# Kernel tuning notes

Measured on AMD Instinct MI355X. Metric: run time of the kernel, lower is better.

The kernel has to match this reference:

```python
import jax, jax.numpy as jnp
import numpy as np

W = 10        # hurst window == signature path window (increments)
DELTA_MAX = 1.5
BN_EPS = 1e-5


def _revcumsum(x, axis):
    return jnp.flip(jnp.cumsum(jnp.flip(x, axis), axis=axis), axis)


def _forward(features, hw1, hb1, hw2, hb2, hw3, hb3, gw1, gb1, gw2, gb2,
             p1, p1b, p2, p2b, p3, p3b, p4, p4b,
             w1, b1, gamma, beta, rmean, rvar, w2, b2, w3, b3):
    B, T, d = features.shape
    f32 = features.dtype
    # log returns, left-padded with 0
    lp = features[:, :, 0]
    ret = jnp.pad(lp[:, 1:] - lp[:, :-1], ((0, 0), (1, 0)))
    # Hurst estimator on sliding windows returns[:, t-W:t] for t in [W, T)
    idxh = jnp.arange(T - W)[:, None] + jnp.arange(W)[None, :]
    rw = ret[:, idxh]                                          # [B, T-W, W]
    hh = jax.nn.relu(rw @ hw1 + hb1)
    hh = jax.nn.relu(hh @ hw2 + hb2)
    H_tail = 0.5 * jax.nn.sigmoid((hh @ hw3 + hb3)[..., 0])    # [B, T-W]
    # first W entries copy the t=W estimate (matches torch slice-broadcast)
    H_local = jnp.concatenate([jnp.repeat(H_tail[:, :1], W, axis=1), H_tail], axis=1)
    vol = jnp.cumsum(jnp.abs(ret), axis=1) / (jnp.arange(1, T + 1, dtype=f32) + 1e-8)
    # depth gate from (H_local, vol_local)
    regime = jnp.stack([H_local, vol], axis=-1)                # [B, T, 2]
    gate = jax.nn.softmax(jax.nn.relu(regime @ gw1 + gb1) @ gw2 + gb2, axis=-1)  # [B,T,4]
    # windowed path increments: window at t covers global increments t-W .. t-1
    Dinc = features[:, 1:] - features[:, :-1]                  # [B, T-1, d]
    Dp = jnp.pad(Dinc, ((0, 0), (W, 0), (0, 0)))
    idx = jnp.arange(T)[:, None] + jnp.arange(W)[None, :]
    Dw = Dp[:, idx]                                            # [B, T, W, d] (zero-padded early)
    S = _revcumsum(Dw, 2)                                      # suffix sums S_r = sum_{m>=r} D_m
    lvl1 = S[:, :, 0]                                          # [B, T, d] = path[-1]-path[0]
    # level2 (torch loop) = sum_{i<=m} D_i (x) D_m  (diagonal included)
    A = Dw[..., :, None] * S[..., None, :]                     # [B, T, W, d, d]
    l2f = jnp.sum(A, axis=2).reshape(B, T, d * d)
    # level3 (torch loop) = sum_{i<j<=n} D_i (x) D_j (x) D_n
    RA = _revcumsum(A, 2) - A                                  # exclusive suffix sum of A
    l3f = jnp.einsum('btrd,btref->btdef', Dw, RA).reshape(B, T, d ** 3)
    # level4 = flatten(level2 (x) level2); (d^2)^2 == d^4 so no pad/trunc
    l4f = (l2f[..., :, None] * l2f[..., None, :]).reshape(B, T, d ** 4)
    proj1 = lvl1 @ p1 + p1b
    proj2 = jnp.concatenate([lvl1, l2f], -1) @ p2 + p2b
    proj3 = jnp.concatenate([lvl1, l2f, l3f], -1) @ p3 + p3b
    proj4 = jnp.concatenate([lvl1, l2f, l3f, l4f], -1) @ p4 + p4b
    # depth k active iff path_len >= k+1 i.e. t >= k (k = depth index)
    tv = jnp.arange(T)
    m2 = (tv >= 1).astype(f32)[None, :, None]
    m3 = (tv >= 2).astype(f32)[None, :, None]
    m4 = (tv >= 3).astype(f32)[None, :, None]
    sig_repr = (gate[..., 0:1] * proj1 + m2 * gate[..., 1:2] * proj2
                + m3 * gate[..., 2:3] * proj3 + m4 * gate[..., 3:4] * proj4)
    combined = jnp.concatenate([sig_repr, features], axis=-1)  # [B, T, h+d]
    h1 = jax.nn.relu(combined @ w1 + b1)
    bn = gamma * (h1 - rmean) * jax.lax.rsqrt(rvar + BN_EPS) + beta  # BatchNorm1d (eval)
    h2 = jax.nn.relu(bn @ w2 + b2)
    return DELTA_MAX * jnp.tanh((h2 @ w3 + b3)[..., 0])        # [B, T]


def setup_inputs() -> dict:
    key = jax.random.key(0)
    ks = jax.random.split(key, 24)
    B, T, d, h = 32, 2048, 5, 64
    def w(k, shape, s=0.1):
        return (jax.random.normal(k, shape) * s).astype(jnp.float32)
    z = lambda n: jnp.zeros((n,), jnp.float32)
    return dict(
        features=0.1 * jax.random.normal(ks[0], (B, T, d), jnp.float32),
        hw1=w(ks[1], (10, 32)), hb1=z(32),
        hw2=w(ks[2], (32, 32)), hb2=z(32),
        hw3=w(ks[3], (32, 1)), hb3=z(1),
        gw1=w(ks[4], (2, 32)), gb1=z(32),
        gw2=w(ks[5], (32, 4)), gb2=z(4),
        p1=w(ks[6], (5, h)), p1b=z(h),
        p2=w(ks[7], (30, h)), p2b=z(h),
        p3=w(ks[8], (155, h)), p3b=z(h),
        p4=w(ks[9], (780, h)), p4b=z(h),
        w1=w(ks[10], (h + d, h)), b1=z(h),
        gamma=jnp.ones((h,), jnp.float32), beta=z(h),
        rmean=0.05 * jax.random.normal(ks[11], (h,), dtype=jnp.float32),
        rvar=jax.random.uniform(ks[12], (h,), jnp.float32, 0.5, 1.5),
        w2=w(ks[13], (h, h // 2)), b2=z(h // 2),
        w3=w(ks[14], (h // 2, 1)), b3=z(1),
    )


def reference(features, hw1, hb1, hw2, hb2, hw3, hb3, gw1, gb1, gw2, gb2,
              p1, p1b, p2, p2b, p3, p3b, p4, p4b,
              w1, b1, gamma, beta, rmean, rvar, w2, b2, w3, b3):
    return _forward(features, hw1, hb1, hw2, hb2, hw3, hb3, gw1, gb1, gw2, gb2,
                    p1, p1b, p2, p2b, p3, p3b, p4, p4b,
                    w1, b1, gamma, beta, rmean, rvar, w2, b2, w3, b3)
```

## Files before the change

kernel.cpp:

```cpp
#include <hip/hip_runtime.h>
#include <math.h>

#define TT 2048
#define W 10

typedef short bf16x8 __attribute__((ext_vector_type(8)));
typedef float f32x4 __attribute__((ext_vector_type(4)));

#define MFMA16(a, b, c) __builtin_amdgcn_mfma_f32_16x16x32_bf16((a), (b), (c), 0, 0, 0)

__device__ __forceinline__ void splitTrunc(float v, unsigned short& hi,
                                           unsigned short& lo) {
  unsigned int u = __float_as_uint(v);
  hi = (unsigned short)(u >> 16);
  float r = v - __uint_as_float(u & 0xffff0000u);
  lo = (unsigned short)(__float_as_uint(r) >> 16);
}

__global__ __launch_bounds__(256) void prep_kernel(
    const float* __restrict__ F, const float* __restrict__ p1,
    const float* __restrict__ p2, const float* __restrict__ p3,
    const float* __restrict__ p4, unsigned short* __restrict__ WtH,
    unsigned short* __restrict__ WtL, float* __restrict__ ret,
    float* __restrict__ vol) {
  const int bid = blockIdx.x, tid = threadIdx.x;
  if (bid >= 32) {
    int g = (bid - 32) * 256 + tid;
    float v;
    if (g < 2048) {
      int h = g >> 5, k = g & 31;
      v = (k < 5) ? p1[k * 64 + h] : 0.f;
    } else if (g < 4096) {
      int loc = g - 2048, h = loc >> 5, k = loc & 31;
      v = (k < 30) ? p2[k * 64 + h] : 0.f;
    } else if (g < 14336) {
      int loc = g - 4096, h = loc / 160, k = loc - h * 160;
      v = (k < 155) ? p3[k * 64 + h] : 0.f;
    } else if (g < 24576) {
      int loc = g - 14336, h = loc / 160, k = loc - h * 160;
      v = (k < 155) ? p4[k * 64 + h] : 0.f;
    } else {
      int loc = g - 24576, row = loc >> 5, j = loc & 31;
      int i = row >> 6, h = row & 63;
      v = (j < 25) ? p4[(155 + i * 25 + j) * 64 + h] : 0.f;
    }
    unsigned short hi, lo;
    splitTrunc(v, hi, lo);
    WtH[g] = hi;
    WtL[g] = lo;
    return;
  }
  __shared__ float sAbs[TT];
  __shared__ float sPart[256];
  const float* fb = F + (size_t)bid * TT * 5;
#pragma unroll
  for (int u = 0; u < 8; ++u) {
    int t = u * 256 + tid;
    float rv = (t > 0) ? (fb[t * 5] - fb[(t - 1) * 5]) : 0.f;
    ret[bid * TT + t] = rv;
    sAbs[t] = fabsf(rv);
  }
  __syncthreads();
  float loc8[8], run = 0.f;
#pragma unroll
  for (int u = 0; u < 8; ++u) {
    run += sAbs[tid * 8 + u];
    loc8[u] = run;
  }
  sPart[tid] = run;
  __syncthreads();
  for (int off = 1; off < 256; off <<= 1) {
    float v = (tid >= off) ? sPart[tid - off] : 0.f;
    __syncthreads();
    sPart[tid] += v;
    __syncthreads();
  }
  float excl = sPart[tid] - run;
#pragma unroll
  for (int u = 0; u < 8; ++u) {
    int t = tid * 8 + u;
    vol[bid * TT + t] = (excl + loc8[u]) / ((float)(t + 1) + 1e-8f);
  }
}

__global__ __launch_bounds__(512, 2) void sig_kernel(
    const float* __restrict__ F, const float* __restrict__ ret_g,
    const float* __restrict__ vol_g, const unsigned short* __restrict__ WtH,
    const unsigned short* __restrict__ WtL, const float* __restrict__ hw1,
    const float* __restrict__ hb1, const float* __restrict__ hw2,
    const float* __restrict__ hb2, const float* __restrict__ hw3,
    const float* __restrict__ hb3, const float* __restrict__ gw1,
    const float* __restrict__ gb1, const float* __restrict__ gw2,
    const float* __restrict__ gb2, const float* __restrict__ p1b,
    const float* __restrict__ p2b, const float* __restrict__ p3b,
    const float* __restrict__ p4b, const float* __restrict__ w1,
    const float* __restrict__ b1, const float* __restrict__ gam,
    const float* __restrict__ bet, const float* __restrict__ rmean,
    const float* __restrict__ rvar, const float* __restrict__ w2,
    const float* __restrict__ b2, const float* __restrict__ w3,
    const float* __restrict__ b3, float* __restrict__ out) {
  __shared__ unsigned short phiH[32][168];
  __shared__ unsigned short phiL[32][168];
  __shared__ unsigned short l2bH[32][40];
  __shared__ unsigned short l2bL[32][40];
  __shared__ float sL2[32 * 25];
  __shared__ __align__(16) float sF[44 * 8];
  __shared__ float retl[42];
  __shared__ float voll[32];
  __shared__ float sGate[32 * 4];
  __shared__ __align__(16) float sU[4352];

  const int tid = threadIdx.x;
  const int b = blockIdx.x >> 6;
  const int t0 = (blockIdx.x & 63) << 5;
  const float* fb = F + (size_t)b * TT * 5;

  for (int u = tid; u < 284; u += 512) {
    if (u < 210) {
      int j = u / 5, ch = u - 5 * j;
      int t = t0 - 10 + j;
      sF[j * 8 + ch] = (t >= 0) ? fb[t * 5 + ch] : 0.f;
    } else if (u < 252) {
      int jj = u - 210;
      int t = t0 - 10 + jj;
      retl[jj] = (t >= 0) ? ret_g[b * TT + t] : 0.f;
    } else {
      int p = u - 252;
      voll[p] = vol_g[b * TT + t0 + p];
    }
  }
  __syncthreads();

  {
    float* sH1 = sU;
    const int p = tid >> 4, q = tid & 15;
    const int t = t0 + p;
    const int soff = (t >= W) ? p : (W - t0);
    float r0[W];
#pragma unroll
    for (int u = 0; u < W; ++u) r0[u] = retl[soff + u];
    const int j = q * 2;
    float ax = hb1[j], ay = hb1[j + 1];
#pragma unroll
    for (int u = 0; u < W; ++u) {
      float2 w = *(const float2*)&hw1[u * 32 + j];
      ax = fmaf(r0[u], w.x, ax);
      ay = fmaf(r0[u], w.y, ay);
    }
    sH1[p * 33 + j] = fmaxf(ax, 0.f);
    sH1[p * 33 + j + 1] = fmaxf(ay, 0.f);
    float bx = hb2[j], by = hb2[j + 1];
    for (int u2 = 0; u2 < 32; ++u2) {
      float hv = sH1[p * 33 + u2];
      float2 w = *(const float2*)&hw2[u2 * 32 + j];
      bx = fmaf(hv, w.x, bx);
      by = fmaf(hv, w.y, by);
    }
    float hsp = fmaxf(bx, 0.f) * hw3[j] + fmaxf(by, 0.f) * hw3[j + 1];
    hsp += __shfl_xor(hsp, 1);
    hsp += __shfl_xor(hsp, 2);
    hsp += __shfl_xor(hsp, 4);
    hsp += __shfl_xor(hsp, 8);
    float H = 0.5f / (1.f + expf(-(hsp + hb3[0])));
    float vv = voll[p];
    float l0 = 0.f, l1 = 0.f, l2v = 0.f, l3v = 0.f;
#pragma unroll
    for (int d = 0; d < 2; ++d) {
      int j3 = q * 2 + d;
      float z = fmaxf(fmaf(H, gw1[j3], fmaf(vv, gw1[32 + j3], gb1[j3])), 0.f);
      l0 = fmaf(z, gw2[j3 * 4 + 0], l0);
      l1 = fmaf(z, gw2[j3 * 4 + 1], l1);
      l2v = fmaf(z, gw2[j3 * 4 + 2], l2v);
      l3v = fmaf(z, gw2[j3 * 4 + 3], l3v);
    }
#pragma unroll
    for (int m = 1; m <= 8; m <<= 1) {
      l0 += __shfl_xor(l0, m);
      l1 += __shfl_xor(l1, m);
      l2v += __shfl_xor(l2v, m);
      l3v += __shfl_xor(l3v, m);
    }
    if (q == 0) {
      l0 += gb2[0]; l1 += gb2[1]; l2v += gb2[2]; l3v += gb2[3];
      float mx = fmaxf(fmaxf(l0, l1), fmaxf(l2v, l3v));
      float e0 = expf(l0 - mx), e1 = expf(l1 - mx);
      float e2 = expf(l2v - mx), e3 = expf(l3v - mx);
      float inv = 1.f / (e0 + e1 + e2 + e3);
      *(float4*)&sGate[p * 4] = make_float4(e0 * inv, e1 * inv, e2 * inv, e3 * inv);
    }
  }

  if (tid < 160) {
    const int p = tid / 5, e = tid - 5 * (tid / 5);
    float aA[5] = {0.f, 0.f, 0.f, 0.f, 0.f};
    float sv[5] = {0.f, 0.f, 0.f, 0.f, 0.f};
    float l3m[5][5];
#pragma unroll
    for (int i = 0; i < 5; ++i)
#pragma unroll
      for (int fi = 0; fi < 5; ++fi) l3m[i][fi] = 0.f;
    float4 c4 = *(const float4*)&sF[(p + 10) * 8];
    float ce = sF[(p + 10) * 8 + 4];
    float cur[5] = {c4.x, c4.y, c4.z, c4.w, ce};
#pragma unroll
    for (int r = 9; r >= 0; --r) {
      float4 n4 = *(const float4*)&sF[(p + r) * 8];
      float ne = sF[(p + r) * 8 + 4];
      float nxt[5] = {n4.x, n4.y, n4.z, n4.w, ne};
      float m = ((t0 != 0) || (p + r >= 10)) ? 1.f : 0.f;
      float d[5];
#pragma unroll
      for (int i = 0; i < 5; ++i) d[i] = (cur[i] - nxt[i]) * m;
#pragma unroll
      for (int fi = 0; fi < 5; ++fi) sv[fi] += d[fi];
#pragma unroll
      for (int i = 0; i < 5; ++i)
#pragma unroll
        for (int fi = 0; fi < 5; ++fi) l3m[i][fi] = fmaf(d[i], aA[fi], l3m[i][fi]);
      float de = (e == 0) ? d[0] : (e == 1) ? d[1] : (e == 2) ? d[2]
                : (e == 3) ? d[3] : d[4];
#pragma unroll
      for (int fi = 0; fi < 5; ++fi) aA[fi] = fmaf(de, sv[fi], aA[fi]);
#pragma unroll
      for (int i = 0; i < 5; ++i) cur[i] = nxt[i];
    }
    unsigned short hi, lo;
#pragma unroll
    for (int fi = 0; fi < 5; ++fi) {
      float a = aA[fi];
      int ef = e * 5 + fi;
      sL2[p * 25 + ef] = a;
      splitTrunc(a, hi, lo);
      phiH[p][5 + ef] = hi;
      phiL[p][5 + ef] = lo;
      l2bH[p][ef] = hi;
      l2bL[p][ef] = lo;
#pragma unroll
      for (int i = 0; i < 5; ++i) {
        splitTrunc(l3m[i][fi], hi, lo);
        phiH[p][30 + i * 25 + ef] = hi;
        phiL[p][30 + i * 25 + ef] = lo;
      }
    }
    if (e == 0) {
#pragma unroll
      for (int i = 0; i < 5; ++i) {
        splitTrunc(sv[i], hi, lo);
        phiH[p][i] = hi;
        phiL[p][i] = lo;
      }
    }
  } else {
    for (int u = tid - 160; u < 384; u += 352) {
      if (u < 160) {
        int p = u / 5, k = 155 + (u - 5 * (u / 5));
        phiH[p][k] = 0;
        phiL[p][k] = 0;
      } else {
        int v = u - 160;
        int p = v / 7, k = 25 + (v - 7 * (v / 7));
        l2bH[p][k] = 0;
        l2bL[p][k] = 0;
      }
    }
  }
  __syncthreads();

  {
    const int lane = tid & 63, wv = tid >> 6;
    const int ptile = wv & 1, htile = wv >> 1;
    const int col = lane & 15, quad = lane >> 4;
    const int pl = ptile * 16 + col;
    const int arow = htile * 16 + col;
    const f32x4 z4 = {0.f, 0.f, 0.f, 0.f};
    f32x4 acc1 = z4, acc2 = z4, acc3a = z4, acc3b = z4;
    f32x4 acc4a = z4, acc4b = z4, acc4c = z4;

    const unsigned short* W4aH = WtH + 14336 + arow * 160 + quad * 8;
    const unsigned short* W4aL = WtL + 14336 + arow * 160 + quad * 8;
    const unsigned short* W3H_ = WtH + 4096 + arow * 160 + quad * 8;
    const unsigned short* W3L_ = WtL + 4096 + arow * 160 + quad * 8;
#pragma unroll
    for (int s = 0; s < 5; ++s) {
      bf16x8 bh = *(const bf16x8*)&phiH[pl][s * 32 + quad * 8];
      bf16x8 bl = *(const bf16x8*)&phiL[pl][s * 32 + quad * 8];
      bf16x8 ah = *(const bf16x8*)(W4aH + s * 32);
      bf16x8 al = *(const bf16x8*)(W4aL + s * 32);
      acc4a = MFMA16(ah, bh, acc4a);
      acc4b = MFMA16(ah, bl, acc4b);
      acc4b = MFMA16(al, bh, acc4b);
      bf16x8 ch = *(const bf16x8*)(W3H_ + s * 32);
      bf16x8 cl = *(const bf16x8*)(W3L_ + s * 32);
      acc3a = MFMA16(ch, bh, acc3a);
      acc3b = MFMA16(ch, bl, acc3b);
      acc3b = MFMA16(cl, bh, acc3b);
      if (s == 0) {
        bf16x8 dh = *(const bf16x8*)(WtH + 2048 + arow * 32 + quad * 8);
        bf16x8 dl = *(const bf16x8*)(WtL + 2048 + arow * 32 + quad * 8);
        acc2 = MFMA16(dh, bh, acc2);
        acc2 = MFMA16(dh, bl, acc2);
        acc2 = MFMA16(dl, bh, acc2);
        bf16x8 eh = *(const bf16x8*)(WtH + arow * 32 + quad * 8);
        bf16x8 el = *(const bf16x8*)(WtL + arow * 32 + quad * 8);
        acc1 = MFMA16(eh, bh, acc1);
        acc1 = MFMA16(eh, bl, acc1);
        acc1 = MFMA16(el, bh, acc1);
      }
    }
    bf16x8 b2h = *(const bf16x8*)&l2bH[pl][quad * 8];
    bf16x8 b2l = *(const bf16x8*)&l2bL[pl][quad * 8];
    const unsigned short* W4bH = WtH + 24576 + arow * 32 + quad * 8;
    const unsigned short* W4bL = WtL + 24576 + arow * 32 + quad * 8;
    const float* l2row = sL2 + pl * 25;
    for (int i = 0; i < 25; ++i) {
      bf16x8 ah = *(const bf16x8*)(W4bH + i * 2048);
      bf16x8 al = *(const bf16x8*)(W4bL + i * 2048);
      f32x4 t4 = MFMA16(ah, b2h, z4);
      t4 = MFMA16(ah, b2l, t4);
      t4 = MFMA16(al, b2h, t4);
      float scl = l2row[i];
      acc4c[0] = fmaf(scl, t4[0], acc4c[0]);
      acc4c[1] = fmaf(scl, t4[1], acc4c[1]);
      acc4c[2] = fmaf(scl, t4[2], acc4c[2]);
      acc4c[3] = fmaf(scl, t4[3], acc4c[3]);
    }
    const int t = t0 + pl;
    float g0 = sGate[pl * 4 + 0];
    float g1 = (t >= 1) ? sGate[pl * 4 + 1] : 0.f;
    float g2 = (t >= 2) ? sGate[pl * 4 + 2] : 0.f;
    float g3 = (t >= 3) ? sGate[pl * 4 + 3] : 0.f;
    float* sSig = sU;
#pragma unroll
    for (int r = 0; r < 4; ++r) {
      int h = htile * 16 + quad * 4 + r;
      float v = g0 * (acc1[r] + p1b[h]) + g1 * (acc2[r] + p2b[h]) +
                g2 * (acc3a[r] + acc3b[r] + p3b[h]) +
                g3 * (acc4a[r] + acc4b[r] + acc4c[r] + p4b[h]);
      sSig[pl * 68 + h] = v;
    }
  }
  __syncthreads();

  {
    const float* sSig = sU;
    float* sBn = sU + 2176;
    const int lane = tid & 63, wv = tid >> 6;
    const int j = lane;
    const int p0 = wv * 4;
    float a0 = b1[j], a1 = a0, a2 = a0, a3 = a0;
    for (int i = 0; i < 64; i += 4) {
      float4 s0 = *(const float4*)&sSig[(p0 + 0) * 68 + i];
      float4 s1 = *(const float4*)&sSig[(p0 + 1) * 68 + i];
      float4 s2 = *(const float4*)&sSig[(p0 + 2) * 68 + i];
      float4 s3 = *(const float4*)&sSig[(p0 + 3) * 68 + i];
      float wa = w1[(i + 0) * 64 + j];
      float wb = w1[(i + 1) * 64 + j];
      float wc = w1[(i + 2) * 64 + j];
      float wd = w1[(i + 3) * 64 + j];
      a0 = fmaf(s0.x, wa, a0); a0 = fmaf(s0.y, wb, a0);
      a0 = fmaf(s0.z, wc, a0); a0 = fmaf(s0.w, wd, a0);
      a1 = fmaf(s1.x, wa, a1); a1 = fmaf(s1.y, wb, a1);
      a1 = fmaf(s1.z, wc, a1); a1 = fmaf(s1.w, wd, a1);
      a2 = fmaf(s2.x, wa, a2); a2 = fmaf(s2.y, wb, a2);
      a2 = fmaf(s2.z, wc, a2); a2 = fmaf(s2.w, wd, a2);
      a3 = fmaf(s3.x, wa, a3); a3 = fmaf(s3.y, wb, a3);
      a3 = fmaf(s3.z, wc, a3); a3 = fmaf(s3.w, wd, a3);
    }
#pragma unroll
    for (int i = 0; i < 5; ++i) {
      float wt = w1[(64 + i) * 64 + j];
      a0 = fmaf(sF[(p0 + 10) * 8 + i], wt, a0);
      a1 = fmaf(sF[(p0 + 11) * 8 + i], wt, a1);
      a2 = fmaf(sF[(p0 + 12) * 8 + i], wt, a2);
      a3 = fmaf(sF[(p0 + 13) * 8 + i], wt, a3);
    }
    float sc = gam[j] * rsqrtf(rvar[j] + 1e-5f);
    float rm = rmean[j], be = bet[j];
    sBn[(p0 + 0) * 68 + j] = fmaf(fmaxf(a0, 0.f) - rm, sc, be);
    sBn[(p0 + 1) * 68 + j] = fmaf(fmaxf(a1, 0.f) - rm, sc, be);
    sBn[(p0 + 2) * 68 + j] = fmaf(fmaxf(a2, 0.f) - rm, sc, be);
    sBn[(p0 + 3) * 68 + j] = fmaf(fmaxf(a3, 0.f) - rm, sc, be);
  }
  __syncthreads();

  {
    const float* sBn = sU + 2176;
    const float b3s = b3[0];
#pragma unroll
    for (int pass = 0; pass < 2; ++pass) {
      int task = tid + pass * 512;
      int p = task >> 5, k = task & 31;
      const float* bnp = sBn + p * 68;
      float a = b2[k];
      for (int jj = 0; jj < 64; jj += 4) {
        float4 bn4 = *(const float4*)&bnp[jj];
        a = fmaf(bn4.x, w2[(jj + 0) * 32 + k], a);
        a = fmaf(bn4.y, w2[(jj + 1) * 32 + k], a);
        a = fmaf(bn4.z, w2[(jj + 2) * 32 + k], a);
        a = fmaf(bn4.w, w2[(jj + 3) * 32 + k], a);
      }
      float partial = fmaxf(a, 0.f) * w3[k];
#pragma unroll
      for (int off = 16; off >= 1; off >>= 1)
        partial += __shfl_xor(partial, off, 32);
      if (k == 0) out[b * TT + t0 + p] = 1.5f * tanhf(partial + b3s);
    }
  }
}

extern "C" void kernel_launch(void* const* d_in, const int* in_sizes, int n_in,
                              void* d_out, int out_size, void* d_ws, size_t ws_size,
                              hipStream_t stream) {
  const float* F = (const float*)d_in[0];
  const float* hw1 = (const float*)d_in[1];
  const float* hb1 = (const float*)d_in[2];
  const float* hw2 = (const float*)d_in[3];
  const float* hb2 = (const float*)d_in[4];
  const float* hw3 = (const float*)d_in[5];
  const float* hb3 = (const float*)d_in[6];
  const float* gw1 = (const float*)d_in[7];
  const float* gb1 = (const float*)d_in[8];
  const float* gw2 = (const float*)d_in[9];
  const float* gb2 = (const float*)d_in[10];
  const float* p1 = (const float*)d_in[11];
  const float* p1b = (const float*)d_in[12];
  const float* p2 = (const float*)d_in[13];
  const float* p2b = (const float*)d_in[14];
  const float* p3 = (const float*)d_in[15];
  const float* p3b = (const float*)d_in[16];
  const float* p4 = (const float*)d_in[17];
  const float* p4b = (const float*)d_in[18];
  const float* w1 = (const float*)d_in[19];
  const float* b1 = (const float*)d_in[20];
  const float* gam = (const float*)d_in[21];
  const float* bet = (const float*)d_in[22];
  const float* rmean = (const float*)d_in[23];
  const float* rvar = (const float*)d_in[24];
  const float* w2 = (const float*)d_in[25];
  const float* b2 = (const float*)d_in[26];
  const float* w3 = (const float*)d_in[27];
  const float* b3 = (const float*)d_in[28];

  float* ws = (float*)d_ws;
  float* ret = ws;
  float* vol = ws + 65536;
  unsigned short* WtH = (unsigned short*)(ws + 131072);
  unsigned short* WtL = WtH + 75776;
  float* out = (float*)d_out;

  prep_kernel<<<328, 256, 0, stream>>>(F, p1, p2, p3, p4, WtH, WtL, ret, vol);
  sig_kernel<<<2048, 512, 0, stream>>>(F, ret, vol, WtH, WtL, hw1, hb1, hw2,
                                       hb2, hw3, hb3, gw1, gb1, gw2, gb2, p1b,
                                       p2b, p3b, p4b, w1, b1, gam, bet, rmean,
                                       rvar, w2, b2, w3, b3, out);
}
```

Baseline: 274.2 us.

## Halve per-block time tile to 16 positions with 256-thread blocks

The signature kernel now processes 16 time steps per block with 256 threads instead of 32 with 512, doubling the grid and halving shared memory per block. The MFMA stage drops the position-tile split so each wave handles one output-feature tile over all 16 positions, and zero-padding of the phi and level-2 buffers moves into the initial load loop. The level-4 inner MFMA chain is split into three independent accumulators to shorten dependency latency. The smaller blocks may raise occupancy and reduce tail effects, but the weight (A operand) loads from global memory are now amortised over half as many positions, roughly doubling weight traffic.

```diff
diff --git a/kernel.cpp b/kernel.cpp
--- a/kernel.cpp
+++ b/kernel.cpp
@@ -83,7 +83,7 @@
   }
 }
 
-__global__ __launch_bounds__(512, 2) void sig_kernel(
+__global__ __launch_bounds__(256, 2) void sig_kernel(
     const float* __restrict__ F, const float* __restrict__ ret_g,
     const float* __restrict__ vol_g, const unsigned short* __restrict__ WtH,
     const unsigned short* __restrict__ WtL, const float* __restrict__ hw1,
@@ -99,34 +99,44 @@
     const float* __restrict__ rvar, const float* __restrict__ w2,
     const float* __restrict__ b2, const float* __restrict__ w3,
     const float* __restrict__ b3, float* __restrict__ out) {
-  __shared__ unsigned short phiH[32][168];
-  __shared__ unsigned short phiL[32][168];
-  __shared__ unsigned short l2bH[32][40];
-  __shared__ unsigned short l2bL[32][40];
-  __shared__ float sL2[32 * 25];
-  __shared__ __align__(16) float sF[44 * 8];
-  __shared__ float retl[42];
-  __shared__ float voll[32];
-  __shared__ float sGate[32 * 4];
-  __shared__ __align__(16) float sU[4352];
+  __shared__ unsigned short phiH[16][168];
+  __shared__ unsigned short phiL[16][168];
+  __shared__ unsigned short l2bH[16][40];
+  __shared__ unsigned short l2bL[16][40];
+  __shared__ float sL2[16 * 25];
+  __shared__ __align__(16) float sF[26 * 8];
+  __shared__ float retl[26];
+  __shared__ float voll[16];
+  __shared__ float sGate[16 * 4];
+  __shared__ __align__(16) float sU[2176];
 
   const int tid = threadIdx.x;
-  const int b = blockIdx.x >> 6;
-  const int t0 = (blockIdx.x & 63) << 5;
+  const int b = blockIdx.x >> 7;
+  const int t0 = (blockIdx.x & 127) << 4;
   const float* fb = F + (size_t)b * TT * 5;
 
-  for (int u = tid; u < 284; u += 512) {
-    if (u < 210) {
+  for (int u = tid; u < 364; u += 256) {
+    if (u < 130) {
       int j = u / 5, ch = u - 5 * j;
       int t = t0 - 10 + j;
       sF[j * 8 + ch] = (t >= 0) ? fb[t * 5 + ch] : 0.f;
-    } else if (u < 252) {
-      int jj = u - 210;
+    } else if (u < 156) {
+      int jj = u - 130;
       int t = t0 - 10 + jj;
       retl[jj] = (t >= 0) ? ret_g[b * TT + t] : 0.f;
+    } else if (u < 172) {
+      int p = u - 156;
+      voll[p] = vol_g[b * TT + t0 + p];
+    } else if (u < 252) {
+      int v = u - 172;
+      int p = v / 5, k = 155 + (v - 5 * (v / 5));
+      phiH[p][k] = 0;
+      phiL[p][k] = 0;
     } else {
-      int p = u - 252;
-      voll[p] = vol_g[b * TT + t0 + p];
+      int v = u - 252;
+      int p = v / 7, k = 25 + (v - 7 * (v / 7));
+      l2bH[p][k] = 0;
+      l2bL[p][k] = 0;
     }
   }
   __syncthreads();
@@ -190,7 +200,7 @@
     }
   }
 
-  if (tid < 160) {
+  if (tid < 80) {
     const int p = tid / 5, e = tid - 5 * (tid / 5);
     float aA[5] = {0.f, 0.f, 0.f, 0.f, 0.f};
     float sv[5] = {0.f, 0.f, 0.f, 0.f, 0.f};
@@ -250,27 +260,13 @@
         phiL[p][i] = lo;
       }
     }
-  } else {
-    for (int u = tid - 160; u < 384; u += 352) {
-      if (u < 160) {
-        int p = u / 5, k = 155 + (u - 5 * (u / 5));
-        phiH[p][k] = 0;
-        phiL[p][k] = 0;
-      } else {
-        int v = u - 160;
-        int p = v / 7, k = 25 + (v - 7 * (v / 7));
-        l2bH[p][k] = 0;
-        l2bL[p][k] = 0;
-      }
-    }
   }
   __syncthreads();
 
   {
-    const int lane = tid & 63, wv = tid >> 6;
-    const int ptile = wv & 1, htile = wv >> 1;
+    const int lane = tid & 63, htile = tid >> 6;
     const int col = lane & 15, quad = lane >> 4;
-    const int pl = ptile * 16 + col;
+    const int pl = col;
     const int arow = htile * 16 + col;
     const f32x4 z4 = {0.f, 0.f, 0.f, 0.f};
     f32x4 acc1 = z4, acc2 = z4, acc3a = z4, acc3b = z4;
@@ -315,14 +311,14 @@
     for (int i = 0; i < 25; ++i) {
       bf16x8 ah = *(const bf16x8*)(W4bH + i * 2048);
       bf16x8 al = *(const bf16x8*)(W4bL + i * 2048);
-      f32x4 t4 = MFMA16(ah, b2h, z4);
-      t4 = MFMA16(ah, b2l, t4);
-      t4 = MFMA16(al, b2h, t4);
+      f32x4 t4a = MFMA16(ah, b2h, z4);
+      f32x4 t4b = MFMA16(ah, b2l, z4);
+      f32x4 t4c = MFMA16(al, b2h, z4);
       float scl = l2row[i];
-      acc4c[0] = fmaf(scl, t4[0], acc4c[0]);
-      acc4c[1] = fmaf(scl, t4[1], acc4c[1]);
-      acc4c[2] = fmaf(scl, t4[2], acc4c[2]);
-      acc4c[3] = fmaf(scl, t4[3], acc4c[3]);
+      acc4c[0] = fmaf(scl, t4a[0] + t4b[0] + t4c[0], acc4c[0]);
+      acc4c[1] = fmaf(scl, t4a[1] + t4b[1] + t4c[1], acc4c[1]);
+      acc4c[2] = fmaf(scl, t4a[2] + t4b[2] + t4c[2], acc4c[2]);
+      acc4c[3] = fmaf(scl, t4a[3] + t4b[3] + t4c[3], acc4c[3]);
     }
     const int t = t0 + pl;
     float g0 = sGate[pl * 4 + 0];
@@ -343,7 +339,7 @@
 
   {
     const float* sSig = sU;
-    float* sBn = sU + 2176;
+    float* sBn = sU + 1088;
     const int lane = tid & 63, wv = tid >> 6;
     const int j = lane;
     const int p0 = wv * 4;
@@ -384,11 +380,11 @@
   __syncthreads();
 
   {
-    const float* sBn = sU + 2176;
+    const float* sBn = sU + 1088;
     const float b3s = b3[0];
 #pragma unroll
     for (int pass = 0; pass < 2; ++pass) {
-      int task = tid + pass * 512;
+      int task = tid + pass * 256;
       int p = task >> 5, k = task & 31;
       const float* bnp = sBn + p * 68;
       float a = b2[k];
@@ -449,7 +445,7 @@
   float* out = (float*)d_out;
 
   prep_kernel<<<328, 256, 0, stream>>>(F, p1, p2, p3, p4, WtH, WtL, ret, vol);
-  sig_kernel<<<2048, 512, 0, stream>>>(F, ret, vol, WtH, WtL, hw1, hb1, hw2,
+  sig_kernel<<<4096, 256, 0, stream>>>(F, ret, vol, WtH, WtL, hw1, hb1, hw2,
                                        hb2, hw3, hb3, gw1, gb1, gw2, gb2, p1b,
                                        p2b, p3b, p4b, w1, b1, gam, bet, rmean,
                                        rvar, w2, b2, w3, b3, out);
```

Result: slower. 371.4 us (+35.5%).
